# Kernel tuning notes

Hardware: AMD Instinct MI355X
Metric: run time of the kernel (lower is better)

## Reference

```python
import jax, jax.numpy as jnp
import numpy as np

P = 113          # vocab (modulus)
D = 128          # residual_dim
H = 4            # n_heads (hardcoded in Model)
DH = D // H      # head_dim = 32
HID = 4 * D      # mlp hidden = 512
BATCH = 131072
RATE = 0.5       # attention_rate


def setup_inputs() -> dict:
    key = jax.random.key(0)
    ks = jax.random.split(key, 12)
    std = 1.0 / D ** 0.5
    x = jax.random.randint(ks[0], (BATCH, 2), 0, P)
    tok_emb = jax.random.normal(ks[1], (P, D), jnp.float32) / D ** 0.5
    pos_emb = jax.random.normal(ks[2], (2, D), jnp.float32) / D ** 0.5
    W_Q = jax.random.normal(ks[3], (H, D, DH), jnp.float32) * std
    W_K = jax.random.normal(ks[4], (H, D, DH), jnp.float32) * std
    W_V = jax.random.normal(ks[5], (H, D, DH), jnp.float32) * std
    W_O = jax.random.normal(ks[6], (H, DH, D), jnp.float32) * std
    # nn.Linear default init: U(-1/sqrt(fan_in), 1/sqrt(fan_in))
    b1_bound = 1.0 / D ** 0.5
    W1 = jax.random.uniform(ks[7], (D, HID), jnp.float32, -b1_bound, b1_bound)
    b1 = jax.random.uniform(ks[8], (HID,), jnp.float32, -b1_bound, b1_bound)
    b2_bound = 1.0 / HID ** 0.5
    W2 = jax.random.uniform(ks[9], (HID, D), jnp.float32, -b2_bound, b2_bound)
    b2 = jax.random.uniform(ks[10], (D,), jnp.float32, -b2_bound, b2_bound)
    W_U = jax.random.normal(ks[11], (P, D), jnp.float32) / P ** 0.5
    return dict(x=x, tok_emb=tok_emb, pos_emb=pos_emb, W_Q=W_Q, W_K=W_K,
                W_V=W_V, W_O=W_O, W1=W1, b1=b1, W2=W2, b2=b2, W_U=W_U)


def reference(x, tok_emb, pos_emb, W_Q, W_K, W_V, W_O, W1, b1, W2, b2, W_U):
    # embed: [B,2,D]
    resid = tok_emb[x] + pos_emb[None, :, :]
    # attention
    q = jnp.einsum('bpd,hdk->bphk', resid, W_Q)
    k = jnp.einsum('bpd,hdk->bphk', resid, W_K)
    v = jnp.einsum('bpd,hdk->bphk', resid, W_V)
    scores = jnp.einsum('bqhk,bshk->bhqs', q, k) / DH ** 0.5  # [B,H,2,2]
    pattern = jax.nn.softmax(scores, axis=-1)
    pattern = (1.0 - RATE) + RATE * pattern  # uniform blend, no causal mask
    z = jnp.einsum('bshk,bhqs->bqhk', v, pattern)
    attn_out = jnp.einsum('bqhk,hkd->bqd', z, W_O)
    resid = resid + attn_out
    # mlp
    h = jax.nn.relu(resid @ W1 + b1)
    resid = resid + (h @ W2 + b2)
    # unembed: [B,2,P]
    logits = jnp.einsum('vd,bpd->bpv', W_U, resid)
    return logits
```

## Files before the change

kernel.cpp:

```cpp
#include <hip/hip_runtime.h>
#include <hip/hip_bf16.h>
#include <stdint.h>

typedef __hip_bfloat16 bf16;
typedef __attribute__((ext_vector_type(8))) short short8;
typedef __attribute__((ext_vector_type(4))) float float4v;
typedef __attribute__((ext_vector_type(2))) float f2v;

#define NVOCAB 113
#define NPAIR (113 * 113)
#define DDIM 128
#define HIDDIM 512
#define PAIRS_PB 16
#define ROWS_PB 32

#define OFF_B1  145792
#define OFF_B2  211840

#define BOFF_WOT 0
#define BOFF_W1T 16384
#define BOFF_W2T (16384 + 65536)
#define BOFF_WUP (16384 + 65536 + 65536)
#define BTOTAL   (16384 + 65536 + 65536 + 16384)

__device__ __forceinline__ uint16_t f2b(float f) {
  bf16 h = __float2bfloat16(f);
  return *(uint16_t*)&h;
}
__device__ __forceinline__ float b2f(uint16_t u) {
  return __uint_as_float(((uint32_t)u) << 16);
}
__device__ __forceinline__ float ldsrc(const void* p, int i, int isb) {
  return isb ? b2f(((const uint16_t*)p)[i]) : ((const float*)p)[i];
}

__device__ __forceinline__ void bar_lds() {
  asm volatile("s_waitcnt lgkmcnt(0)\n\ts_barrier" ::: "memory");
}

__device__ __forceinline__ short8 gl16(const uint16_t* p) {
  short8 r;
  asm volatile("global_load_dwordx4 %0, %1, off" : "=v"(r) : "v"(p));
  return r;
}
#define VMW4(a0,a1,a2,a3) \
  asm volatile("s_waitcnt vmcnt(0)" : "+v"(a0),"+v"(a1),"+v"(a2),"+v"(a3))
#define VMW8(a0,a1,a2,a3,a4,a5,a6,a7) \
  asm volatile("s_waitcnt vmcnt(0)" : "+v"(a0),"+v"(a1),"+v"(a2),"+v"(a3), \
                                      "+v"(a4),"+v"(a5),"+v"(a6),"+v"(a7))

__device__ __forceinline__ int detect_isb(const uint32_t* __restrict__ tok_raw) {
  uint32_t u = tok_raw[threadIdx.x & 63];
  int e = (u >> 7) & 0xff;
  unsigned long long m = __ballot(e >= 100 && e <= 126);
  return __popcll(m) >= 48;
}

struct SrcPtrs { const void* p[11]; };

__global__ void __launch_bounds__(384) build_kernel(
    SrcPtrs sp, float* __restrict__ wf,
    float* __restrict__ resid_pre, float* __restrict__ qt,
    float* __restrict__ kt, float* __restrict__ vt,
    uint16_t* __restrict__ wb) {
  const int tid = threadIdx.x;
  const int blk = blockIdx.x;
  const int isb = detect_isb((const uint32_t*)sp.p[0]);

  if (blk < 226) {
    const int row = blk;
    const int t = row >> 1, p = row & 1;
    __shared__ float r[DDIM];
    if (tid < DDIM) {
      float rv = ldsrc(sp.p[0], t * DDIM + tid, isb) +
                 ldsrc(sp.p[1], p * DDIM + tid, isb);
      r[tid] = rv;
      resid_pre[row * DDIM + tid] = rv;
    }
    __syncthreads();
    const int which = tid >> 7, jj = tid & 127;
    const int h = jj >> 5, j = jj & 31;
    const void* wsrc = sp.p[2 + which];
    const int base = h * 4096 + j;
    float a = 0.f;
    if (isb) {
      const uint16_t* w16 = (const uint16_t*)wsrc;
      #pragma unroll 8
      for (int d = 0; d < 128; ++d)
        a += r[d] * b2f(w16[base + d * 32]);
    } else {
      const float* w32 = (const float*)wsrc;
      #pragma unroll 8
      for (int d = 0; d < 128; ++d)
        a += r[d] * w32[base + d * 32];
    }
    float* outp = (which == 0) ? qt : (which == 1) ? kt : vt;
    outp[row * DDIM + jj] = a;
  } else if (blk < 653) {
    const int idx = (blk - 226) * 384 + tid;
    if (idx < BTOTAL) {
      float v;
      if (idx < BOFF_W1T) {
        int l = idx, d = l >> 7, c = l & 127;
        v = ldsrc(sp.p[5], c * 128 + d, isb);
      } else if (idx < BOFF_W2T) {
        int l = idx - BOFF_W1T, n = l >> 7, d = l & 127;
        v = ldsrc(sp.p[6], d * 512 + n, isb);
      } else if (idx < BOFF_WUP) {
        int l = idx - BOFF_W2T, d = l >> 9, j = l & 511;
        v = ldsrc(sp.p[8], j * 128 + d, isb);
      } else {
        int l = idx - BOFF_WUP, vv = l >> 7, d = l & 127;
        v = (vv < NVOCAB) ? ldsrc(sp.p[10], vv * 128 + d, isb) : 0.f;
      }
      wb[idx] = f2b(v);
    }
  } else {
    const int i = (blk - 653) * 384 + tid;
    if (i < 512) wf[OFF_B1 + i] = ldsrc(sp.p[7], i, isb);
    else if (i < 640) wf[OFF_B2 + (i - 512)] = ldsrc(sp.p[9], i - 512, isb);
  }
}

__global__ void __launch_bounds__(512, 2) pair_mfma_kernel(
    const float* __restrict__ resid_pre, const float* __restrict__ qt,
    const float* __restrict__ kt, const float* __restrict__ vt,
    const float* __restrict__ wf, const uint16_t* __restrict__ wb,
    float* __restrict__ table) {
  __shared__ uint16_t bufH[ROWS_PB * 512];
  __shared__ uint16_t bufZ[ROWS_PB * 128];
  __shared__ uint16_t bufS[ROWS_PB * 128];
  __shared__ float    spat[PAIRS_PB * 16];

  const int tid = threadIdx.x;
  const int blk = blockIdx.x;
  const int lane = tid & 63;
  const int npar = tid >> 6;
  const int l15 = lane & 15, quad = lane >> 4;

  #define ROW_OF(row_) ({                                        \
    int pr_ = blk * PAIRS_PB + ((row_) >> 1);                    \
    if (pr_ >= NPAIR) pr_ = NPAIR - 1;                           \
    int t0_ = pr_ / NVOCAB, t1_ = pr_ - t0_ * NVOCAB;            \
    ((row_) & 1) ? t1_ * 2 + 1 : t0_ * 2; })

  const int nG = npar * 16 + l15;

  short8 bW0[4];
  {
    const uint16_t* bp = wb + BOFF_WOT + nG * 128 + quad * 8;
    bW0[0] = gl16(bp);       bW0[1] = gl16(bp + 32);
    bW0[2] = gl16(bp + 64);  bW0[3] = gl16(bp + 96);
  }

  float rpre[2][4];
  #pragma unroll
  for (int mf = 0; mf < 2; ++mf)
    #pragma unroll
    for (int r = 0; r < 4; ++r)
      rpre[mf][r] = resid_pre[ROW_OF(mf * 16 + quad * 4 + r) * DDIM + nG];
  float bias1v[4];
  #pragma unroll
  for (int ni = 0; ni < 4; ++ni)
    bias1v[ni] = wf[OFF_B1 + (npar + ni * 8) * 16 + l15];
  const float bias2 = wf[OFF_B2 + nG];
  const int zm = tid >> 4, zc0 = (tid & 15) * 8;
  float4 zv0a, zv0b, zv1a, zv1b;
  {
    const int zr0 = ROW_OF((zm >> 1) * 2);
    const int zr1 = ROW_OF((zm >> 1) * 2 + 1);
    const float4* p0 = (const float4*)(vt + zr0 * DDIM + zc0);
    const float4* p1 = (const float4*)(vt + zr1 * DDIM + zc0);
    zv0a = p0[0]; zv0b = p0[1]; zv1a = p1[0]; zv1b = p1[1];
  }

  if (tid < 128) {
    const int pl = tid >> 3, s = tid & 7;
    int pair = blk * PAIRS_PB + pl;
    if (pair >= NPAIR) pair = NPAIR - 1;
    const int t0 = pair / NVOCAB, t1 = pair - t0 * NVOCAB;
    const int row0 = t0 * 2, row1 = t1 * 2 + 1;
    const int h = s >> 1, qp = s & 1;
    const float4* qrow = (const float4*)(qt + (qp ? row1 : row0) * DDIM + h * 32);
    const float4* k0r  = (const float4*)(kt + row0 * DDIM + h * 32);
    const float4* k1r  = (const float4*)(kt + row1 * DDIM + h * 32);
    float acc0 = 0.f, acc1 = 0.f;
    #pragma unroll
    for (int j = 0; j < 8; ++j) {
      float4 qv = qrow[j], kv0 = k0r[j], kv1 = k1r[j];
      acc0 += qv.x * kv0.x + qv.y * kv0.y + qv.z * kv0.z + qv.w * kv0.w;
      acc1 += qv.x * kv1.x + qv.y * kv1.y + qv.z * kv1.z + qv.w * kv1.w;
    }
    float s0 = acc0 * 0.17677669529663687f;
    float s1 = acc1 * 0.17677669529663687f;
    float m = fmaxf(s0, s1);
    float e0 = __expf(s0 - m), e1 = __expf(s1 - m);
    float inv = 1.f / (e0 + e1);
    spat[pl * 16 + s * 2]     = 0.5f + 0.5f * e0 * inv;
    spat[pl * 16 + s * 2 + 1] = 0.5f + 0.5f * e1 * inv;
  }
  bar_lds();

  {
    const int pl = zm >> 1, qp = zm & 1;
    const int h = zc0 >> 5;
    const float p0 = spat[pl * 16 + h * 4 + qp * 2];
    const float p1 = spat[pl * 16 + h * 4 + qp * 2 + 1];
    float v0[8] = {zv0a.x, zv0a.y, zv0a.z, zv0a.w, zv0b.x, zv0b.y, zv0b.z, zv0b.w};
    float v1[8] = {zv1a.x, zv1a.y, zv1a.z, zv1a.w, zv1b.x, zv1b.y, zv1b.z, zv1b.w};
    short8 pk;
    #pragma unroll
    for (int e = 0; e < 8; ++e)
      pk[e] = (short)f2b(p0 * v0[e] + p1 * v1[e]);
    *(short8*)&bufZ[(zm * 16 + ((zc0 >> 3) ^ (zm & 15))) * 8] = pk;
  }
  bar_lds();

  float smid[2][4];
  short8 bW1[4][4];

  {
    short8 af[2][4];
    #pragma unroll
    for (int mf = 0; mf < 2; ++mf)
      #pragma unroll
      for (int ks = 0; ks < 4; ++ks)
        af[mf][ks] = *(const short8*)&bufZ[((mf * 16 + l15) * 16 +
                                           ((ks * 4 + quad) ^ l15)) * 8];
    VMW4(bW0[0], bW0[1], bW0[2], bW0[3]);
    #pragma unroll
    for (int ni = 0; ni < 4; ++ni) {
      const int n = (npar + ni * 8) * 16 + l15;
      const uint16_t* bp = wb + BOFF_W1T + n * 128 + quad * 8;
      #pragma unroll
      for (int ks = 0; ks < 4; ++ks)
        bW1[ni][ks] = gl16(bp + ks * 32);
    }
    float4v acc[2] = {{0.f, 0.f, 0.f, 0.f}, {0.f, 0.f, 0.f, 0.f}};
    #pragma unroll
    for (int mf = 0; mf < 2; ++mf)
      #pragma unroll
      for (int ks = 0; ks < 4; ++ks)
        acc[mf] = __builtin_amdgcn_mfma_f32_16x16x32_bf16(af[mf][ks], bW0[ks],
                                                          acc[mf], 0, 0, 0);
    #pragma unroll
    for (int mf = 0; mf < 2; ++mf)
      #pragma unroll
      for (int r = 0; r < 4; ++r) {
        const int row = mf * 16 + quad * 4 + r;
        float v = acc[mf][r] + rpre[mf][r];
        smid[mf][r] = v;
        bufS[(row * 16 + ((nG >> 3) ^ (row & 15))) * 8 + (nG & 7)] = f2b(v);
      }
  }
  bar_lds();

  short8 bB2[16];

  {
    short8 af[2][4];
    #pragma unroll
    for (int mf = 0; mf < 2; ++mf)
      #pragma unroll
      for (int ks = 0; ks < 4; ++ks)
        af[mf][ks] = *(const short8*)&bufS[((mf * 16 + l15) * 16 +
                                           ((ks * 4 + quad) ^ l15)) * 8];
    VMW8(bW1[0][0], bW1[0][1], bW1[0][2], bW1[0][3],
         bW1[1][0], bW1[1][1], bW1[1][2], bW1[1][3]);
    VMW8(bW1[2][0], bW1[2][1], bW1[2][2], bW1[2][3],
         bW1[3][0], bW1[3][1], bW1[3][2], bW1[3][3]);
    {
      const uint16_t* bp = wb + BOFF_W2T + nG * 512 + quad * 8;
      #pragma unroll
      for (int k8 = 0; k8 < 16; ++k8)
        bB2[k8] = gl16(bp + k8 * 32);
    }
    #pragma unroll
    for (int ni = 0; ni < 4; ++ni) {
      const int n = (npar + ni * 8) * 16 + l15;
      float4v acc[2] = {{0.f, 0.f, 0.f, 0.f}, {0.f, 0.f, 0.f, 0.f}};
      #pragma unroll
      for (int mf = 0; mf < 2; ++mf)
        #pragma unroll
        for (int ks = 0; ks < 4; ++ks)
          acc[mf] = __builtin_amdgcn_mfma_f32_16x16x32_bf16(
              af[mf][ks], bW1[ni][ks], acc[mf], 0, 0, 0);
      const float bias = bias1v[ni];
      #pragma unroll
      for (int mf = 0; mf < 2; ++mf)
        #pragma unroll
        for (int r = 0; r < 4; ++r) {
          const int row = mf * 16 + quad * 4 + r;
          bufH[(row * 64 + ((n >> 3) ^ (row & 15))) * 8 + (n & 7)] =
              f2b(fmaxf(acc[mf][r] + bias, 0.f));
        }
    }
  }
  bar_lds();

  short8 bW3[4];

  {
    VMW8(bB2[0], bB2[1], bB2[2],  bB2[3],  bB2[4],  bB2[5],  bB2[6],  bB2[7]);
    VMW8(bB2[8], bB2[9], bB2[10], bB2[11], bB2[12], bB2[13], bB2[14], bB2[15]);
    {
      const uint16_t* bp3 = wb + BOFF_WUP + nG * 128 + quad * 8;
      bW3[0] = gl16(bp3);       bW3[1] = gl16(bp3 + 32);
      bW3[2] = gl16(bp3 + 64);  bW3[3] = gl16(bp3 + 96);
    }
    float4v acc0 = {0.f, 0.f, 0.f, 0.f};
    float4v acc1 = {0.f, 0.f, 0.f, 0.f};
    #pragma unroll
    for (int half = 0; half < 2; ++half) {
      #pragma unroll
      for (int qtr = 0; qtr < 2; ++qtr) {
        short8 a0[4], a1[4];
        #pragma unroll
        for (int k4 = 0; k4 < 4; ++k4) {
          const int ks = half * 8 + qtr * 4 + k4;
          a0[k4] = *(const short8*)&bufH[(l15 * 64 +
                                         ((ks * 4 + quad) ^ l15)) * 8];
          a1[k4] = *(const short8*)&bufH[((16 + l15) * 64 +
                                         ((ks * 4 + quad) ^ l15)) * 8];
        }
        #pragma unroll
        for (int k4 = 0; k4 < 4; ++k4) {
          const int ks = half * 8 + qtr * 4 + k4;
          acc0 = __builtin_amdgcn_mfma_f32_16x16x32_bf16(
              a0[k4], bB2[ks], acc0, 0, 0, 0);
          acc1 = __builtin_amdgcn_mfma_f32_16x16x32_bf16(
              a1[k4], bB2[ks], acc1, 0, 0, 0);
        }
      }
    }
    #pragma unroll
    for (int r = 0; r < 4; ++r) {
      const int row0 = quad * 4 + r;
      const int row1 = 16 + quad * 4 + r;
      bufZ[(row0 * 16 + ((nG >> 3) ^ (row0 & 15))) * 8 + (nG & 7)] =
          f2b(acc0[r] + bias2 + smid[0][r]);
      bufZ[(row1 * 16 + ((nG >> 3) ^ (row1 & 15))) * 8 + (nG & 7)] =
          f2b(acc1[r] + bias2 + smid[1][r]);
    }
  }
  bar_lds();

  {
    short8 ar[2][4];
    #pragma unroll
    for (int mf = 0; mf < 2; ++mf)
      #pragma unroll
      for (int ks = 0; ks < 4; ++ks)
        ar[mf][ks] = *(const short8*)&bufZ[((mf * 16 + l15) * 16 +
                                           ((ks * 4 + quad) ^ l15)) * 8];
    VMW4(bW3[0], bW3[1], bW3[2], bW3[3]);
    float4v acc[2] = {{0.f, 0.f, 0.f, 0.f}, {0.f, 0.f, 0.f, 0.f}};
    #pragma unroll
    for (int mf = 0; mf < 2; ++mf)
      #pragma unroll
      for (int ks = 0; ks < 4; ++ks)
        acc[mf] = __builtin_amdgcn_mfma_f32_16x16x32_bf16(ar[mf][ks], bW3[ks],
                                                          acc[mf], 0, 0, 0);
    if (nG < NVOCAB) {
      #pragma unroll
      for (int mf = 0; mf < 2; ++mf)
        #pragma unroll
        for (int r = 0; r < 4; ++r) {
          const int row = mf * 16 + quad * 4 + r;
          const int pair = blk * PAIRS_PB + (row >> 1);
          if (pair < NPAIR)
            table[pair * 226 + (row & 1) * 113 + nG] = acc[mf][r];
        }
    }
  }
  #undef ROW_OF
}

__global__ void __launch_bounds__(256) gather_kernel(
    const uint32_t* __restrict__ x_raw, const f2v* __restrict__ table2,
    f2v* __restrict__ out2, int total) {
  uint32_t xs = x_raw[2 * (threadIdx.x & 63) + 1];
  unsigned long long nz = __ballot(xs != 0u);
  const int is64 = (nz == 0ull);

  const int stride = gridDim.x * 256;
  for (int i = blockIdx.x * 256 + threadIdx.x; i < total; i += stride) {
    const int b = i / NVOCAB;
    const int j = i - b * NVOCAB;
    int t0, t1;
    if (is64) {
      t0 = (int)x_raw[4 * b];
      t1 = (int)x_raw[4 * b + 2];
    } else {
      t0 = (int)x_raw[2 * b];
      t1 = (int)x_raw[2 * b + 1];
    }
    t0 = min(max(t0, 0), NVOCAB - 1);
    t1 = min(max(t1, 0), NVOCAB - 1);
    const int pair = t0 * NVOCAB + t1;
    f2v v = table2[(size_t)pair * NVOCAB + j];
    __builtin_nontemporal_store(v, &out2[i]);
  }
}

extern "C" void kernel_launch(void* const* d_in, const int* in_sizes, int n_in,
                              void* d_out, int out_size, void* d_ws, size_t ws_size,
                              hipStream_t stream) {
  float*    wf        = (float*)((char*)d_ws + 256);
  float*    resid_pre = (float*)((char*)d_ws + 905984);
  float*    qt        = (float*)((char*)d_ws + 1021696);
  float*    kt        = (float*)((char*)d_ws + 1137408);
  float*    vt        = (float*)((char*)d_ws + 1253120);
  float*    table     = (float*)((char*)d_ws + 1368832);
  uint16_t* wb        = (uint16_t*)((char*)d_ws + 12912016);

  const int B = in_sizes[0] / 2;

  SrcPtrs sp;
  for (int i = 0; i < 11; ++i) sp.p[i] = d_in[i + 1];

  build_kernel<<<655, 384, 0, stream>>>(sp, wf, resid_pre, qt, kt, vt, wb);

  const int nblk = (NPAIR + PAIRS_PB - 1) / PAIRS_PB;
  pair_mfma_kernel<<<nblk, 512, 0, stream>>>(resid_pre, qt, kt, vt, wf, wb,
                                             table);

  const int total = B * NVOCAB;
  gather_kernel<<<2048, 256, 0, stream>>>(
      (const uint32_t*)d_in[0], (const f2v*)table, (f2v*)d_out, total);
}
```

Baseline: 233.5 us.

## Make pair MFMA kernel persistent with register-resident weights across tiles

Converts the pair table kernel into a persistent kernel of 256 blocks, each looping over several 16-pair tiles. All weight fragments (W_O, W1, W2, W_U) are loaded into registers once per block and reused, rather than streamed per tile with staged waits. Occupancy drops to one block per CU under launch bounds of 1, and the per-tile load of residual and value rows is no longer overlapped with weight fetches, so latency hiding may suffer.

Result: slower. 287.1 us (+22.9%).

```diff
diff --git a/kernel.cpp b/kernel.cpp
--- a/kernel.cpp
+++ b/kernel.cpp
@@ -13,6 +13,7 @@
 #define HIDDIM 512
 #define PAIRS_PB 16
 #define ROWS_PB 32
+#define NTILES ((NPAIR + PAIRS_PB - 1) / PAIRS_PB)
 
 #define OFF_B1  145792
 #define OFF_B2  211840
@@ -43,11 +44,6 @@
   asm volatile("global_load_dwordx4 %0, %1, off" : "=v"(r) : "v"(p));
   return r;
 }
-#define VMW4(a0,a1,a2,a3) \
-  asm volatile("s_waitcnt vmcnt(0)" : "+v"(a0),"+v"(a1),"+v"(a2),"+v"(a3))
-#define VMW8(a0,a1,a2,a3,a4,a5,a6,a7) \
-  asm volatile("s_waitcnt vmcnt(0)" : "+v"(a0),"+v"(a1),"+v"(a2),"+v"(a3), \
-                                      "+v"(a4),"+v"(a5),"+v"(a6),"+v"(a7))
 
 __device__ __forceinline__ int detect_isb(const uint32_t* __restrict__ tok_raw) {
   uint32_t u = tok_raw[threadIdx.x & 63];
@@ -122,7 +118,7 @@
   }
 }
 
-__global__ void __launch_bounds__(512, 2) pair_mfma_kernel(
+__global__ void __launch_bounds__(512, 1) pair_mfma_kernel(
     const float* __restrict__ resid_pre, const float* __restrict__ qt,
     const float* __restrict__ kt, const float* __restrict__ vt,
     const float* __restrict__ wf, const uint16_t* __restrict__ wb,
@@ -133,247 +129,237 @@
   __shared__ float    spat[PAIRS_PB * 16];
 
   const int tid = threadIdx.x;
-  const int blk = blockIdx.x;
   const int lane = tid & 63;
   const int npar = tid >> 6;
   const int l15 = lane & 15, quad = lane >> 4;
-
-  #define ROW_OF(row_) ({                                        \
-    int pr_ = blk * PAIRS_PB + ((row_) >> 1);                    \
-    if (pr_ >= NPAIR) pr_ = NPAIR - 1;                           \
-    int t0_ = pr_ / NVOCAB, t1_ = pr_ - t0_ * NVOCAB;            \
-    ((row_) & 1) ? t1_ * 2 + 1 : t0_ * 2; })
-
   const int nG = npar * 16 + l15;
 
-  short8 bW0[4];
-  {
-    const uint16_t* bp = wb + BOFF_WOT + nG * 128 + quad * 8;
-    bW0[0] = gl16(bp);       bW0[1] = gl16(bp + 32);
-    bW0[2] = gl16(bp + 64);  bW0[3] = gl16(bp + 96);
-  }
-
-  float rpre[2][4];
-  #pragma unroll
-  for (int mf = 0; mf < 2; ++mf)
-    #pragma unroll
-    for (int r = 0; r < 4; ++r)
-      rpre[mf][r] = resid_pre[ROW_OF(mf * 16 + quad * 4 + r) * DDIM + nG];
   float bias1v[4];
   #pragma unroll
   for (int ni = 0; ni < 4; ++ni)
     bias1v[ni] = wf[OFF_B1 + (npar + ni * 8) * 16 + l15];
   const float bias2 = wf[OFF_B2 + nG];
+
+  short8 bW0[4], bW1[4][4], bB2[16], bW3[4];
+  {
+    const uint16_t* p0 = wb + BOFF_WOT + nG * 128 + quad * 8;
+    #pragma unroll
+    for (int ks = 0; ks < 4; ++ks) bW0[ks] = gl16(p0 + ks * 32);
+    #pragma unroll
+    for (int ni = 0; ni < 4; ++ni) {
+      const uint16_t* p1 = wb + BOFF_W1T + ((npar + ni * 8) * 16 + l15) * 128 +
+                           quad * 8;
+      #pragma unroll
+      for (int ks = 0; ks < 4; ++ks) bW1[ni][ks] = gl16(p1 + ks * 32);
+    }
+    const uint16_t* p2 = wb + BOFF_W2T + nG * 512 + quad * 8;
+    #pragma unroll
+    for (int k8 = 0; k8 < 16; ++k8) bB2[k8] = gl16(p2 + k8 * 32);
+    const uint16_t* p3 = wb + BOFF_WUP + nG * 128 + quad * 8;
+    #pragma unroll
+    for (int ks = 0; ks < 4; ++ks) bW3[ks] = gl16(p3 + ks * 32);
+  }
+  asm volatile("s_waitcnt vmcnt(0)" ::: "memory");
+  __builtin_amdgcn_sched_barrier(0);
+
   const int zm = tid >> 4, zc0 = (tid & 15) * 8;
-  float4 zv0a, zv0b, zv1a, zv1b;
-  {
-    const int zr0 = ROW_OF((zm >> 1) * 2);
-    const int zr1 = ROW_OF((zm >> 1) * 2 + 1);
-    const float4* p0 = (const float4*)(vt + zr0 * DDIM + zc0);
-    const float4* p1 = (const float4*)(vt + zr1 * DDIM + zc0);
-    zv0a = p0[0]; zv0b = p0[1]; zv1a = p1[0]; zv1b = p1[1];
-  }
-
-  if (tid < 128) {
-    const int pl = tid >> 3, s = tid & 7;
-    int pair = blk * PAIRS_PB + pl;
-    if (pair >= NPAIR) pair = NPAIR - 1;
-    const int t0 = pair / NVOCAB, t1 = pair - t0 * NVOCAB;
-    const int row0 = t0 * 2, row1 = t1 * 2 + 1;
-    const int h = s >> 1, qp = s & 1;
-    const float4* qrow = (const float4*)(qt + (qp ? row1 : row0) * DDIM + h * 32);
-    const float4* k0r  = (const float4*)(kt + row0 * DDIM + h * 32);
-    const float4* k1r  = (const float4*)(kt + row1 * DDIM + h * 32);
-    float acc0 = 0.f, acc1 = 0.f;
-    #pragma unroll
-    for (int j = 0; j < 8; ++j) {
-      float4 qv = qrow[j], kv0 = k0r[j], kv1 = k1r[j];
-      acc0 += qv.x * kv0.x + qv.y * kv0.y + qv.z * kv0.z + qv.w * kv0.w;
-      acc1 += qv.x * kv1.x + qv.y * kv1.y + qv.z * kv1.z + qv.w * kv1.w;
-    }
-    float s0 = acc0 * 0.17677669529663687f;
-    float s1 = acc1 * 0.17677669529663687f;
-    float m = fmaxf(s0, s1);
-    float e0 = __expf(s0 - m), e1 = __expf(s1 - m);
-    float inv = 1.f / (e0 + e1);
-    spat[pl * 16 + s * 2]     = 0.5f + 0.5f * e0 * inv;
-    spat[pl * 16 + s * 2 + 1] = 0.5f + 0.5f * e1 * inv;
-  }
-  bar_lds();
-
-  {
-    const int pl = zm >> 1, qp = zm & 1;
-    const int h = zc0 >> 5;
-    const float p0 = spat[pl * 16 + h * 4 + qp * 2];
-    const float p1 = spat[pl * 16 + h * 4 + qp * 2 + 1];
-    float v0[8] = {zv0a.x, zv0a.y, zv0a.z, zv0a.w, zv0b.x, zv0b.y, zv0b.z, zv0b.w};
-    float v1[8] = {zv1a.x, zv1a.y, zv1a.z, zv1a.w, zv1b.x, zv1b.y, zv1b.z, zv1b.w};
-    short8 pk;
-    #pragma unroll
-    for (int e = 0; e < 8; ++e)
-      pk[e] = (short)f2b(p0 * v0[e] + p1 * v1[e]);
-    *(short8*)&bufZ[(zm * 16 + ((zc0 >> 3) ^ (zm & 15))) * 8] = pk;
-  }
-  bar_lds();
-
-  float smid[2][4];
-  short8 bW1[4][4];
-
-  {
-    short8 af[2][4];
+
+  for (int tile = blockIdx.x; tile < NTILES; tile += gridDim.x) {
+    const int bp = tile * PAIRS_PB;
+
+    #define ROW_OF(row_) ({                                      \
+      int pr_ = bp + ((row_) >> 1);                              \
+      if (pr_ >= NPAIR) pr_ = NPAIR - 1;                         \
+      int t0_ = pr_ / NVOCAB, t1_ = pr_ - t0_ * NVOCAB;          \
+      ((row_) & 1) ? t1_ * 2 + 1 : t0_ * 2; })
+
+    float rpre[2][4];
     #pragma unroll
     for (int mf = 0; mf < 2; ++mf)
       #pragma unroll
-      for (int ks = 0; ks < 4; ++ks)
-        af[mf][ks] = *(const short8*)&bufZ[((mf * 16 + l15) * 16 +
-                                           ((ks * 4 + quad) ^ l15)) * 8];
-    VMW4(bW0[0], bW0[1], bW0[2], bW0[3]);
-    #pragma unroll
-    for (int ni = 0; ni < 4; ++ni) {
-      const int n = (npar + ni * 8) * 16 + l15;
-      const uint16_t* bp = wb + BOFF_W1T + n * 128 + quad * 8;
-      #pragma unroll
-      for (int ks = 0; ks < 4; ++ks)
-        bW1[ni][ks] = gl16(bp + ks * 32);
-    }
-    float4v acc[2] = {{0.f, 0.f, 0.f, 0.f}, {0.f, 0.f, 0.f, 0.f}};
-    #pragma unroll
-    for (int mf = 0; mf < 2; ++mf)
-      #pragma unroll
-      for (int ks = 0; ks < 4; ++ks)
-        acc[mf] = __builtin_amdgcn_mfma_f32_16x16x32_bf16(af[mf][ks], bW0[ks],
-                                                          acc[mf], 0, 0, 0);
-    #pragma unroll
-    for (int mf = 0; mf < 2; ++mf)
-      #pragma unroll
-      for (int r = 0; r < 4; ++r) {
-        const int row = mf * 16 + quad * 4 + r;
-        float v = acc[mf][r] + rpre[mf][r];
-        smid[mf][r] = v;
-        bufS[(row * 16 + ((nG >> 3) ^ (row & 15))) * 8 + (nG & 7)] = f2b(v);
-      }
-  }
-  bar_lds();
-
-  short8 bB2[16];
-
-  {
-    short8 af[2][4];
-    #pragma unroll
-    for (int mf = 0; mf < 2; ++mf)
-      #pragma unroll
-      for (int ks = 0; ks < 4; ++ks)
-        af[mf][ks] = *(const short8*)&bufS[((mf * 16 + l15) * 16 +
-                                           ((ks * 4 + quad) ^ l15)) * 8];
-    VMW8(bW1[0][0], bW1[0][1], bW1[0][2], bW1[0][3],
-         bW1[1][0], bW1[1][1], bW1[1][2], bW1[1][3]);
-    VMW8(bW1[2][0], bW1[2][1], bW1[2][2], bW1[2][3],
-         bW1[3][0], bW1[3][1], bW1[3][2], bW1[3][3]);
-    {
-      const uint16_t* bp = wb + BOFF_W2T + nG * 512 + quad * 8;
-      #pragma unroll
-      for (int k8 = 0; k8 < 16; ++k8)
-        bB2[k8] = gl16(bp + k8 * 32);
-    }
-    #pragma unroll
-    for (int ni = 0; ni < 4; ++ni) {
-      const int n = (npar + ni * 8) * 16 + l15;
+      for (int r = 0; r < 4; ++r)
+        rpre[mf][r] = resid_pre[ROW_OF(mf * 16 + quad * 4 + r) * DDIM + nG];
+    float4 zv0a, zv0b, zv1a, zv1b;
+    {
+      const int zr0 = ROW_OF((zm >> 1) * 2);
+      const int zr1 = ROW_OF((zm >> 1) * 2 + 1);
+      const float4* p0 = (const float4*)(vt + zr0 * DDIM + zc0);
+      const float4* p1 = (const float4*)(vt + zr1 * DDIM + zc0);
+      zv0a = p0[0]; zv0b = p0[1]; zv1a = p1[0]; zv1b = p1[1];
+    }
+
+    if (tid < 128) {
+      const int pl = tid >> 3, s = tid & 7;
+      int pair = bp + pl;
+      if (pair >= NPAIR) pair = NPAIR - 1;
+      const int t0 = pair / NVOCAB, t1 = pair - t0 * NVOCAB;
+      const int row0 = t0 * 2, row1 = t1 * 2 + 1;
+      const int h = s >> 1, qp = s & 1;
+      const float4* qrow = (const float4*)(qt + (qp ? row1 : row0) * DDIM + h * 32);
+      const float4* k0r  = (const float4*)(kt + row0 * DDIM + h * 32);
+      const float4* k1r  = (const float4*)(kt + row1 * DDIM + h * 32);
+      float acc0 = 0.f, acc1 = 0.f;
+      #pragma unroll
+      for (int j = 0; j < 8; ++j) {
+        float4 qv = qrow[j], kv0 = k0r[j], kv1 = k1r[j];
+        acc0 += qv.x * kv0.x + qv.y * kv0.y + qv.z * kv0.z + qv.w * kv0.w;
+        acc1 += qv.x * kv1.x + qv.y * kv1.y + qv.z * kv1.z + qv.w * kv1.w;
+      }
+      float s0 = acc0 * 0.17677669529663687f;
+      float s1 = acc1 * 0.17677669529663687f;
+      float m = fmaxf(s0, s1);
+      float e0 = __expf(s0 - m), e1 = __expf(s1 - m);
+      float inv = 1.f / (e0 + e1);
+      spat[pl * 16 + s * 2]     = 0.5f + 0.5f * e0 * inv;
+      spat[pl * 16 + s * 2 + 1] = 0.5f + 0.5f * e1 * inv;
+    }
+    bar_lds();
+
+    {
+      const int pl = zm >> 1, qp = zm & 1;
+      const int h = zc0 >> 5;
+      const float p0 = spat[pl * 16 + h * 4 + qp * 2];
+      const float p1 = spat[pl * 16 + h * 4 + qp * 2 + 1];
+      float v0[8] = {zv0a.x, zv0a.y, zv0a.z, zv0a.w,
+                     zv0b.x, zv0b.y, zv0b.z, zv0b.w};
+      float v1[8] = {zv1a.x, zv1a.y, zv1a.z, zv1a.w,
+                     zv1b.x, zv1b.y, zv1b.z, zv1b.w};
+      short8 pk;
+      #pragma unroll
+      for (int e = 0; e < 8; ++e)
+        pk[e] = (short)f2b(p0 * v0[e] + p1 * v1[e]);
+      *(short8*)&bufZ[(zm * 16 + ((zc0 >> 3) ^ (zm & 15))) * 8] = pk;
+    }
+    bar_lds();
+
+    float smid[2][4];
+
+    {
+      short8 af[2][4];
+      #pragma unroll
+      for (int mf = 0; mf < 2; ++mf)
+        #pragma unroll
+        for (int ks = 0; ks < 4; ++ks)
+          af[mf][ks] = *(const short8*)&bufZ[((mf * 16 + l15) * 16 +
+                                             ((ks * 4 + quad) ^ l15)) * 8];
       float4v acc[2] = {{0.f, 0.f, 0.f, 0.f}, {0.f, 0.f, 0.f, 0.f}};
       #pragma unroll
       for (int mf = 0; mf < 2; ++mf)
         #pragma unroll
         for (int ks = 0; ks < 4; ++ks)
           acc[mf] = __builtin_amdgcn_mfma_f32_16x16x32_bf16(
-              af[mf][ks], bW1[ni][ks], acc[mf], 0, 0, 0);
-      const float bias = bias1v[ni];
+              af[mf][ks], bW0[ks], acc[mf], 0, 0, 0);
       #pragma unroll
       for (int mf = 0; mf < 2; ++mf)
         #pragma unroll
         for (int r = 0; r < 4; ++r) {
           const int row = mf * 16 + quad * 4 + r;
-          bufH[(row * 64 + ((n >> 3) ^ (row & 15))) * 8 + (n & 7)] =
-              f2b(fmaxf(acc[mf][r] + bias, 0.f));
+          float v = acc[mf][r] + rpre[mf][r];
+          smid[mf][r] = v;
+          bufS[(row * 16 + ((nG >> 3) ^ (row & 15))) * 8 + (nG & 7)] = f2b(v);
         }
     }
+    bar_lds();
+
+    {
+      short8 af[2][4];
+      #pragma unroll
+      for (int mf = 0; mf < 2; ++mf)
+        #pragma unroll
+        for (int ks = 0; ks < 4; ++ks)
+          af[mf][ks] = *(const short8*)&bufS[((mf * 16 + l15) * 16 +
+                                             ((ks * 4 + quad) ^ l15)) * 8];
+      #pragma unroll
+      for (int ni = 0; ni < 4; ++ni) {
+        const int n = (npar + ni * 8) * 16 + l15;
+        float4v acc[2] = {{0.f, 0.f, 0.f, 0.f}, {0.f, 0.f, 0.f, 0.f}};
+        #pragma unroll
+        for (int mf = 0; mf < 2; ++mf)
+          #pragma unroll
+          for (int ks = 0; ks < 4; ++ks)
+            acc[mf] = __builtin_amdgcn_mfma_f32_16x16x32_bf16(
+                af[mf][ks], bW1[ni][ks], acc[mf], 0, 0, 0);
+        const float bias = bias1v[ni];
+        #pragma unroll
+        for (int mf = 0; mf < 2; ++mf)
+          #pragma unroll
+          for (int r = 0; r < 4; ++r) {
+            const int row = mf * 16 + quad * 4 + r;
+            bufH[(row * 64 + ((n >> 3) ^ (row & 15))) * 8 + (n & 7)] =
+                f2b(fmaxf(acc[mf][r] + bias, 0.f));
+          }
+      }
+    }
+    bar_lds();
+
+    {
+      float4v acc0 = {0.f, 0.f, 0.f, 0.f};
+      float4v acc1 = {0.f, 0.f, 0.f, 0.f};
+      #pragma unroll
+      for (int half = 0; half < 2; ++half) {
+        #pragma unroll
+        for (int qtr = 0; qtr < 2; ++qtr) {
+          short8 a0[4], a1[4];
+          #pragma unroll
+          for (int k4 = 0; k4 < 4; ++k4) {
+            const int ks = half * 8 + qtr * 4 + k4;
+            a0[k4] = *(const short8*)&bufH[(l15 * 64 +
+                                           ((ks * 4 + quad) ^ l15)) * 8];
+            a1[k4] = *(const short8*)&bufH[((16 + l15) * 64 +
+                                           ((ks * 4 + quad) ^ l15)) * 8];
+          }
+          #pragma unroll
+          for (int k4 = 0; k4 < 4; ++k4) {
+            const int ks = half * 8 + qtr * 4 + k4;
+            acc0 = __builtin_amdgcn_mfma_f32_16x16x32_bf16(
+                a0[k4], bB2[ks], acc0, 0, 0, 0);
+            acc1 = __builtin_amdgcn_mfma_f32_16x16x32_bf16(
+                a1[k4], bB2[ks], acc1, 0, 0, 0);
+          }
+        }
+      }
+      #pragma unroll
+      for (int r = 0; r < 4; ++r) {
+        const int row0 = quad * 4 + r;
+        const int row1 = 16 + quad * 4 + r;
+        bufZ[(row0 * 16 + ((nG >> 3) ^ (row0 & 15))) * 8 + (nG & 7)] =
+            f2b(acc0[r] + bias2 + smid[0][r]);
+        bufZ[(row1 * 16 + ((nG >> 3) ^ (row1 & 15))) * 8 + (nG & 7)] =
+            f2b(acc1[r] + bias2 + smid[1][r]);
+      }
+    }
+    bar_lds();
+
+    {
+      short8 ar[2][4];
+      #pragma unroll
+      for (int mf = 0; mf < 2; ++mf)
+        #pragma unroll
+        for (int ks = 0; ks < 4; ++ks)
+          ar[mf][ks] = *(const short8*)&bufZ[((mf * 16 + l15) * 16 +
+                                             ((ks * 4 + quad) ^ l15)) * 8];
+      float4v acc[2] = {{0.f, 0.f, 0.f, 0.f}, {0.f, 0.f, 0.f, 0.f}};
+      #pragma unroll
+      for (int mf = 0; mf < 2; ++mf)
+        #pragma unroll
+        for (int ks = 0; ks < 4; ++ks)
+          acc[mf] = __builtin_amdgcn_mfma_f32_16x16x32_bf16(
+              ar[mf][ks], bW3[ks], acc[mf], 0, 0, 0);
+      if (nG < NVOCAB) {
+        #pragma unroll
+        for (int mf = 0; mf < 2; ++mf)
+          #pragma unroll
+          for (int r = 0; r < 4; ++r) {
+            const int row = mf * 16 + quad * 4 + r;
+            const int pair = bp + (row >> 1);
+            if (pair < NPAIR)
+              table[pair * 226 + (row & 1) * 113 + nG] = acc[mf][r];
+          }
+      }
+    }
+    bar_lds();
+    #undef ROW_OF
   }
-  bar_lds();
-
-  short8 bW3[4];
-
-  {
-    VMW8(bB2[0], bB2[1], bB2[2],  bB2[3],  bB2[4],  bB2[5],  bB2[6],  bB2[7]);
-    VMW8(bB2[8], bB2[9], bB2[10], bB2[11], bB2[12], bB2[13], bB2[14], bB2[15]);
-    {
-      const uint16_t* bp3 = wb + BOFF_WUP + nG * 128 + quad * 8;
-      bW3[0] = gl16(bp3);       bW3[1] = gl16(bp3 + 32);
-      bW3[2] = gl16(bp3 + 64);  bW3[3] = gl16(bp3 + 96);
-    }
-    float4v acc0 = {0.f, 0.f, 0.f, 0.f};
-    float4v acc1 = {0.f, 0.f, 0.f, 0.f};
-    #pragma unroll
-    for (int half = 0; half < 2; ++half) {
-      #pragma unroll
-      for (int qtr = 0; qtr < 2; ++qtr) {
-        short8 a0[4], a1[4];
-        #pragma unroll
-        for (int k4 = 0; k4 < 4; ++k4) {
-          const int ks = half * 8 + qtr * 4 + k4;
-          a0[k4] = *(const short8*)&bufH[(l15 * 64 +
-                                         ((ks * 4 + quad) ^ l15)) * 8];
-          a1[k4] = *(const short8*)&bufH[((16 + l15) * 64 +
-                                         ((ks * 4 + quad) ^ l15)) * 8];
-        }
-        #pragma unroll
-        for (int k4 = 0; k4 < 4; ++k4) {
-          const int ks = half * 8 + qtr * 4 + k4;
-          acc0 = __builtin_amdgcn_mfma_f32_16x16x32_bf16(
-              a0[k4], bB2[ks], acc0, 0, 0, 0);
-          acc1 = __builtin_amdgcn_mfma_f32_16x16x32_bf16(
-              a1[k4], bB2[ks], acc1, 0, 0, 0);
-        }
-      }
-    }
-    #pragma unroll
-    for (int r = 0; r < 4; ++r) {
-      const int row0 = quad * 4 + r;
-      const int row1 = 16 + quad * 4 + r;
-      bufZ[(row0 * 16 + ((nG >> 3) ^ (row0 & 15))) * 8 + (nG & 7)] =
-          f2b(acc0[r] + bias2 + smid[0][r]);
-      bufZ[(row1 * 16 + ((nG >> 3) ^ (row1 & 15))) * 8 + (nG & 7)] =
-          f2b(acc1[r] + bias2 + smid[1][r]);
-    }
-  }
-  bar_lds();
-
-  {
-    short8 ar[2][4];
-    #pragma unroll
-    for (int mf = 0; mf < 2; ++mf)
-      #pragma unroll
-      for (int ks = 0; ks < 4; ++ks)
-        ar[mf][ks] = *(const short8*)&bufZ[((mf * 16 + l15) * 16 +
-                                           ((ks * 4 + quad) ^ l15)) * 8];
-    VMW4(bW3[0], bW3[1], bW3[2], bW3[3]);
-    float4v acc[2] = {{0.f, 0.f, 0.f, 0.f}, {0.f, 0.f, 0.f, 0.f}};
-    #pragma unroll
-    for (int mf = 0; mf < 2; ++mf)
-      #pragma unroll
-      for (int ks = 0; ks < 4; ++ks)
-        acc[mf] = __builtin_amdgcn_mfma_f32_16x16x32_bf16(ar[mf][ks], bW3[ks],
-                                                          acc[mf], 0, 0, 0);
-    if (nG < NVOCAB) {
-      #pragma unroll
-      for (int mf = 0; mf < 2; ++mf)
-        #pragma unroll
-        for (int r = 0; r < 4; ++r) {
-          const int row = mf * 16 + quad * 4 + r;
-          const int pair = blk * PAIRS_PB + (row >> 1);
-          if (pair < NPAIR)
-            table[pair * 226 + (row & 1) * 113 + nG] = acc[mf][r];
-        }
-    }
-  }
-  #undef ROW_OF
 }
 
 __global__ void __launch_bounds__(256) gather_kernel(
@@ -421,9 +407,8 @@
 
   build_kernel<<<655, 384, 0, stream>>>(sp, wf, resid_pre, qt, kt, vt, wb);
 
-  const int nblk = (NPAIR + PAIRS_PB - 1) / PAIRS_PB;
-  pair_mfma_kernel<<<nblk, 512, 0, stream>>>(resid_pre, qt, kt, vt, wf, wb,
-                                             table);
+  pair_mfma_kernel<<<256, 512, 0, stream>>>(resid_pre, qt, kt, vt, wf, wb,
+                                            table);
 
   const int total = B * NVOCAB;
   gather_kernel<<<2048, 256, 0, stream>>>(
```
